# Optimization experiments

Hardware: AMD Instinct MI355X
Metric: run time of the kernel (lower is better)

Reference implementation:

```python
import jax, jax.numpy as jnp
import numpy as np

D_MODEL = 1024


def setup_inputs() -> dict:
    key = jax.random.key(0)
    ks = jax.random.split(key, 8)
    B, S, D = 32, 2048, D_MODEL
    scale = 1.0 / np.sqrt(D)
    return {
        "query": jax.random.normal(ks[0], (B, D), dtype=jnp.float32),
        "keys": jax.random.normal(ks[1], (B, S, D), dtype=jnp.float32),
        "Wq_w": jax.random.normal(ks[2], (D, D), dtype=jnp.float32) * scale,
        "Wq_b": jax.random.normal(ks[3], (D,), dtype=jnp.float32) * 0.01,
        "Wk_w": jax.random.normal(ks[4], (D, D), dtype=jnp.float32) * scale,
        "Wk_b": jax.random.normal(ks[5], (D,), dtype=jnp.float32) * 0.01,
        "v_w": jax.random.normal(ks[6], (D,), dtype=jnp.float32) * scale,
        "v_b": jax.random.normal(ks[7], (1,), dtype=jnp.float32) * 0.01,
    }


def reference(query, keys, Wq_w, Wq_b, Wk_w, Wk_b, v_w, v_b):
    # q: [B, 1, D], k: [B, S, D]
    q = (query @ Wq_w.T + Wq_b)[:, None, :]
    k = keys @ Wk_w.T + Wk_b
    # additive (Bahdanau) scores: [B, S]
    scores = jnp.einsum("bsd,d->bs", jnp.tanh(q + k), v_w) + v_b[0]
    attn = jax.nn.softmax(scores, axis=-1)
    # weighted sum over original keys: [B, D]
    context = jnp.einsum("bs,bsd->bd", attn, keys)
    return (context, attn)
```

## Files before the change

### kernel.cpp

```cpp
#include <hip/hip_runtime.h>
#include <cstddef>
#include <cstdint>

#define BATCH 32
#define SEQ 2048
#define DM 1024

typedef __attribute__((ext_vector_type(8))) _Float16 half8v;
typedef __attribute__((ext_vector_type(4))) _Float16 half4v;
typedef __attribute__((ext_vector_type(2))) __fp16 fp16x2;
typedef __attribute__((ext_vector_type(4))) float f32x4;

__device__ _Float16 g_Bpk[8 * 8 * 32 * 4 * 16 * 8];
__device__ float g_q[BATCH * DM];
__device__ float g_sp[8][BATCH * SEQ];

__device__ __forceinline__ float tanh_fast(float x) {
    float e = __expf(2.0f * x);
    return 1.0f - 2.0f / (e + 1.0f);
}

__global__ __launch_bounds__(256) void packb_kernel(const float* __restrict__ Wk_w) {
    int blk = blockIdx.x;
    int nc = blk >> 3, sub = blk & 7;
    int t = threadIdx.x;
    int row = t & 15, kgrp = (t >> 4) & 3, kt0 = t >> 6;
    const float* src = Wk_w + (size_t)(nc * 128 + sub * 16 + row) * DM;
    _Float16* dst = g_Bpk + (size_t)blk * 16384;
#pragma unroll
    for (int pass = 0; pass < 8; ++pass) {
        int kt = pass * 4 + kt0;
        float4 w0 = *reinterpret_cast<const float4*>(src + kt * 32 + kgrp * 8);
        float4 w1 = *reinterpret_cast<const float4*>(src + kt * 32 + kgrp * 8 + 4);
        union { _Float16 f[8]; half8v v; } h;
        h.f[0] = (_Float16)w0.x; h.f[1] = (_Float16)w0.y;
        h.f[2] = (_Float16)w0.z; h.f[3] = (_Float16)w0.w;
        h.f[4] = (_Float16)w1.x; h.f[5] = (_Float16)w1.y;
        h.f[6] = (_Float16)w1.z; h.f[7] = (_Float16)w1.w;
        *reinterpret_cast<half8v*>(&dst[(size_t)((kt * 4 + kgrp) * 16 + row) * 8]) = h.v;
    }
}

__global__ __launch_bounds__(256) void init_kernel(float* __restrict__ context) {
    int idx = blockIdx.x * 256 + threadIdx.x;
    if (idx < BATCH * DM) context[idx] = 0.f;
}

__global__ __launch_bounds__(256) void qproj_kernel(const float* __restrict__ query,
                                                    const float* __restrict__ Wq_w,
                                                    const float* __restrict__ Wq_b) {
    int d = blockIdx.x;
    int t = threadIdx.x;
    __shared__ float wrow[DM];
    __shared__ float part[8][32];
    reinterpret_cast<float4*>(wrow)[t] =
        reinterpret_cast<const float4*>(Wq_w + (size_t)d * DM)[t];
    __syncthreads();
    int b = t & 31, seg = t >> 5;
    const float4* qp = reinterpret_cast<const float4*>(query + b * DM + seg * 128);
    const float4* wp = reinterpret_cast<const float4*>(wrow + seg * 128);
    float acc = 0.f;
#pragma unroll
    for (int i = 0; i < 32; ++i) {
        float4 qv = qp[i];
        float4 wv = wp[i];
        acc += qv.x * wv.x + qv.y * wv.y + qv.z * wv.z + qv.w * wv.w;
    }
    part[seg][b] = acc;
    __syncthreads();
    if (t < 32) {
        float s = Wq_b[d];
#pragma unroll
        for (int g = 0; g < 8; ++g) s += part[g][t];
        g_q[t * DM + d] = s;
    }
}

#define BM 128
#define BN 256
#define NT2 16

__global__ __launch_bounds__(256, 2) void scores_kernel(const float* __restrict__ keys,
                                                        const float* __restrict__ Wk_b,
                                                        const float* __restrict__ v_w) {
    __shared__ _Float16 AhS[2][2][4][BM + 1][8];

    const unsigned bid = blockIdx.x;
    const unsigned L = (bid & 7u) * 256u + (bid >> 3);
    const int mtile = (int)(L >> 2);
    const int nchunk = (int)(L & 3u);
    const int m0 = mtile * BM;
    const int b = m0 >> 11;

    const int t = threadIdx.x;
    const int w = t >> 6, l = t & 63;
    const int wm = w >> 1, wn = w & 1;
    const int lr = l & 15, lg = l >> 4;

    const int akc = (l & 7) >> 1;
    const int aoff = ((l & 7) & 1) * 4;
    const float* Ap = keys + (size_t)(m0 + w * 32 + (l >> 3)) * DM + (l & 7) * 4;

    const int oldnc = nchunk * 2 + wn;
    const _Float16* Bp = g_Bpk + (size_t)oldnc * 8 * 16384
                               + (size_t)(l >> 4) * 128 + (size_t)(l & 15) * 8;

    float4 as0[4], as1[4];
    half8v bE[8], bO[8];

    f32x4 acc[4][8];
#pragma unroll
    for (int mi = 0; mi < 4; ++mi)
#pragma unroll
        for (int ni = 0; ni < 8; ++ni)
#pragma unroll
            for (int c = 0; c < 4; ++c) acc[mi][ni][c] = 0.f;

#define LOAD_A2(kt)                                                              \
    {                                                                            \
        _Pragma("unroll") for (int j = 0; j < 4; ++j)                            \
            as0[j] = *reinterpret_cast<const float4*>(                           \
                Ap + (size_t)j * 8 * DM + (kt) * 64);                            \
        _Pragma("unroll") for (int j = 0; j < 4; ++j)                            \
            as1[j] = *reinterpret_cast<const float4*>(                           \
                Ap + (size_t)j * 8 * DM + (kt) * 64 + 32);                       \
    }
#define LOAD_BF(ks, dst)                                                         \
    {                                                                            \
        _Pragma("unroll") for (int ni = 0; ni < 8; ++ni)                         \
            dst[ni] = *reinterpret_cast<const half8v*>(                          \
                Bp + (size_t)ni * 16384 + (size_t)(ks) * 512);                   \
    }
#define STAGE_ONE(bufi, sub, areg)                                               \
    {                                                                            \
        _Pragma("unroll") for (int j = 0; j < 4; ++j) {                          \
            const float* fa = reinterpret_cast<const float*>(&areg[j]);          \
            union { fp16x2 h2[2]; half4v v; } u;                                 \
            u.h2[0] = __builtin_amdgcn_cvt_pkrtz(fa[0], fa[1]);                  \
            u.h2[1] = __builtin_amdgcn_cvt_pkrtz(fa[2], fa[3]);                  \
            *reinterpret_cast<half4v*>(                                          \
                &AhS[bufi][sub][akc][w * 32 + j * 8 + (l >> 3)][aoff]) = u.v;    \
        }                                                                        \
    }
#define COMPUTE_S(bufi, sub, breg)                                               \
    {                                                                            \
        __builtin_amdgcn_s_setprio(1);                                           \
        _Pragma("unroll") for (int mi = 0; mi < 4; ++mi) {                       \
            half8v ahv = *reinterpret_cast<const half8v*>(                       \
                &AhS[bufi][sub][lg][wm * 64 + mi * 16 + lr][0]);                 \
            _Pragma("unroll") for (int ni = 0; ni < 8; ++ni)                     \
                acc[mi][ni] = __builtin_amdgcn_mfma_f32_16x16x32_f16(            \
                    ahv, breg[ni], acc[mi][ni], 0, 0, 0);                        \
        }                                                                        \
        __builtin_amdgcn_s_setprio(0);                                          \
    }
#define SYNC()                                                                   \
    asm volatile("s_waitcnt lgkmcnt(0)" ::: "memory");                           \
    __builtin_amdgcn_s_barrier();                                                \
    asm volatile("" ::: "memory");

    LOAD_A2(0);
    LOAD_BF(0, bE);
    STAGE_ONE(0, 0, as0);
    STAGE_ONE(0, 1, as1);
    SYNC()

    for (int tt = 0; tt < NT2; ++tt) {
        const int cb = tt & 1;
        LOAD_BF(2 * tt + 1, bO);
        if (tt + 1 < NT2) LOAD_A2(tt + 1);
        COMPUTE_S(cb, 0, bE);
        COMPUTE_S(cb, 1, bO);
        if (tt + 1 < NT2) {
            STAGE_ONE(cb ^ 1, 0, as0);
            STAGE_ONE(cb ^ 1, 1, as1);
            LOAD_BF(2 * tt + 2, bE);
        }
        SYNC()
    }

    float qb[8], vw[8];
#pragma unroll
    for (int ni = 0; ni < 8; ++ni) {
        int n = oldnc * 128 + ni * 16 + lr;
        qb[ni] = g_q[b * DM + n] + Wk_b[n];
        vw[ni] = v_w[n];
    }
#pragma unroll
    for (int mi = 0; mi < 4; ++mi) {
#pragma unroll
        for (int rg = 0; rg < 4; ++rg) {
            float p = 0.f;
#pragma unroll
            for (int ni = 0; ni < 8; ++ni) {
                float val = acc[mi][ni][rg] + qb[ni];
                p += tanh_fast(val) * vw[ni];
            }
#pragma unroll
            for (int off = 8; off >= 1; off >>= 1) p += __shfl_xor(p, off, 16);
            if (lr == 0)
                g_sp[oldnc][m0 + wm * 64 + mi * 16 + lg * 4 + rg] = p;
        }
    }
#undef LOAD_A2
#undef LOAD_BF
#undef STAGE_ONE
#undef COMPUTE_S
#undef SYNC
}

__global__ __launch_bounds__(256) void softmax_kernel(float* __restrict__ attn) {
    int b = blockIdx.x;
    int tid = threadIdx.x;
    __shared__ float redm[4];
    __shared__ float reds[4];
    float v[8];
    float mx = -1e30f;
#pragma unroll
    for (int i = 0; i < 8; ++i) {
        int idx = b * SEQ + i * 256 + tid;
        float s = 0.f;
#pragma unroll
        for (int pslot = 0; pslot < 8; ++pslot) s += g_sp[pslot][idx];
        v[i] = s;
        mx = fmaxf(mx, v[i]);
    }
#pragma unroll
    for (int off = 32; off >= 1; off >>= 1) mx = fmaxf(mx, __shfl_xor(mx, off));
    int wid = tid >> 6;
    if ((tid & 63) == 0) redm[wid] = mx;
    __syncthreads();
    mx = fmaxf(fmaxf(redm[0], redm[1]), fmaxf(redm[2], redm[3]));
    float sum = 0.f;
#pragma unroll
    for (int i = 0; i < 8; ++i) {
        v[i] = expf(v[i] - mx);
        sum += v[i];
    }
#pragma unroll
    for (int off = 32; off >= 1; off >>= 1) sum += __shfl_xor(sum, off);
    if ((tid & 63) == 0) reds[wid] = sum;
    __syncthreads();
    sum = reds[0] + reds[1] + reds[2] + reds[3];
    float inv = 1.f / sum;
#pragma unroll
    for (int i = 0; i < 8; ++i) attn[b * SEQ + i * 256 + tid] = v[i] * inv;
}

__global__ __launch_bounds__(256) void context_kernel(const float* __restrict__ keys,
                                                      const float* __restrict__ attn,
                                                      float* __restrict__ context) {
    int id = blockIdx.x;
    int schunk = id & 15;
    int b = id >> 4;
    int tid = threadIdx.x;
    __shared__ float a_s[128];
    if (tid < 128) a_s[tid] = attn[b * SEQ + schunk * 128 + tid];
    __syncthreads();
    const float4* kp =
        reinterpret_cast<const float4*>(keys + ((size_t)b * SEQ + schunk * 128) * DM) + tid;
    float4 acc = {0.f, 0.f, 0.f, 0.f};
#pragma unroll 4
    for (int s = 0; s < 128; ++s) {
        float4 kv = kp[(size_t)s * (DM / 4)];
        float a = a_s[s];
        acc.x += a * kv.x; acc.y += a * kv.y; acc.z += a * kv.z; acc.w += a * kv.w;
    }
    atomicAdd(&context[b * DM + tid * 4 + 0], acc.x);
    atomicAdd(&context[b * DM + tid * 4 + 1], acc.y);
    atomicAdd(&context[b * DM + tid * 4 + 2], acc.z);
    atomicAdd(&context[b * DM + tid * 4 + 3], acc.w);
}

extern "C" void kernel_launch(void* const* d_in, const int* in_sizes, int n_in,
                              void* d_out, int out_size, void* d_ws, size_t ws_size,
                              hipStream_t stream) {
    const float* query = (const float*)d_in[0];
    const float* keys  = (const float*)d_in[1];
    const float* Wq_w  = (const float*)d_in[2];
    const float* Wq_b  = (const float*)d_in[3];
    const float* Wk_w  = (const float*)d_in[4];
    const float* Wk_b  = (const float*)d_in[5];
    const float* v_w   = (const float*)d_in[6];

    float* context = (float*)d_out;
    float* attn    = context + BATCH * DM;

    hipLaunchKernelGGL(packb_kernel, dim3(64), dim3(256), 0, stream, Wk_w);
    hipLaunchKernelGGL(init_kernel, dim3(128), dim3(256), 0, stream, context);
    hipLaunchKernelGGL(qproj_kernel, dim3(DM), dim3(256), 0, stream, query, Wq_w, Wq_b);
    hipLaunchKernelGGL(scores_kernel, dim3((BATCH * SEQ / BM) * (DM / BN)), dim3(256), 0, stream,
                       keys, Wk_b, v_w);
    hipLaunchKernelGGL(softmax_kernel, dim3(BATCH), dim3(256), 0, stream, attn);
    hipLaunchKernelGGL(context_kernel, dim3(512), dim3(256), 0, stream, keys, attn, context);
}
```

Measured before the change: 236.9 us.

## Switch scores GEMM to 32x32x16 MFMA with repacked B layout

Replaces the 16x16x32 f16 MFMA tiles in the scores GEMM with 32x32x16 MFMA tiles, so each wave holds 2x4 accumulators of 16 floats instead of 4x8 of 4. The packed Wk layout, the LDS A layout and the epilogue row mapping are rewritten to match. B fragments are now four rotating register sets loaded in the gaps between compute steps. The aim is fewer LDS A reads per MFMA and a higher-throughput MFMA shape, at the cost of more B global loads per k-tile and a new epilogue shuffle pattern.

```diff
diff --git a/kernel.cpp b/kernel.cpp
--- a/kernel.cpp
+++ b/kernel.cpp
@@ -9,9 +9,9 @@
 typedef __attribute__((ext_vector_type(8))) _Float16 half8v;
 typedef __attribute__((ext_vector_type(4))) _Float16 half4v;
 typedef __attribute__((ext_vector_type(2))) __fp16 fp16x2;
-typedef __attribute__((ext_vector_type(4))) float f32x4;
-
-__device__ _Float16 g_Bpk[8 * 8 * 32 * 4 * 16 * 8];
+typedef __attribute__((ext_vector_type(16))) float f32x16;
+
+__device__ _Float16 g_Bpk[8 * 4 * 64 * 64 * 8];
 __device__ float g_q[BATCH * DM];
 __device__ float g_sp[8][BATCH * SEQ];
 
@@ -22,22 +22,27 @@
 
 __global__ __launch_bounds__(256) void packb_kernel(const float* __restrict__ Wk_w) {
     int blk = blockIdx.x;
-    int nc = blk >> 3, sub = blk & 7;
+    int oldnc = blk >> 3, kq = blk & 7;
     int t = threadIdx.x;
-    int row = t & 15, kgrp = (t >> 4) & 3, kt0 = t >> 6;
-    const float* src = Wk_w + (size_t)(nc * 128 + sub * 16 + row) * DM;
-    _Float16* dst = g_Bpk + (size_t)blk * 16384;
-#pragma unroll
-    for (int pass = 0; pass < 8; ++pass) {
-        int kt = pass * 4 + kt0;
-        float4 w0 = *reinterpret_cast<const float4*>(src + kt * 32 + kgrp * 8);
-        float4 w1 = *reinterpret_cast<const float4*>(src + kt * 32 + kgrp * 8 + 4);
-        union { _Float16 f[8]; half8v v; } h;
-        h.f[0] = (_Float16)w0.x; h.f[1] = (_Float16)w0.y;
-        h.f[2] = (_Float16)w0.z; h.f[3] = (_Float16)w0.w;
-        h.f[4] = (_Float16)w1.x; h.f[5] = (_Float16)w1.y;
-        h.f[6] = (_Float16)w1.z; h.f[7] = (_Float16)w1.w;
-        *reinterpret_cast<half8v*>(&dst[(size_t)((kt * 4 + kgrp) * 16 + row) * 8]) = h.v;
+    int w = t >> 6, l = t & 63;
+    int c32 = l & 31, khalf = l >> 5;
+#pragma unroll
+    for (int ni = 0; ni < 4; ++ni) {
+#pragma unroll
+        for (int s = 0; s < 2; ++s) {
+            int ks = kq * 8 + w * 2 + s;
+            const float* src = Wk_w + (size_t)(oldnc * 128 + ni * 32 + c32) * DM
+                             + ks * 16 + khalf * 8;
+            float4 f0 = *reinterpret_cast<const float4*>(src);
+            float4 f1 = *reinterpret_cast<const float4*>(src + 4);
+            union { fp16x2 h2[4]; half8v v; } u;
+            u.h2[0] = __builtin_amdgcn_cvt_pkrtz(f0.x, f0.y);
+            u.h2[1] = __builtin_amdgcn_cvt_pkrtz(f0.z, f0.w);
+            u.h2[2] = __builtin_amdgcn_cvt_pkrtz(f1.x, f1.y);
+            u.h2[3] = __builtin_amdgcn_cvt_pkrtz(f1.z, f1.w);
+            *reinterpret_cast<half8v*>(
+                &g_Bpk[(((size_t)(oldnc * 4 + ni) * 64 + ks) * 64 + l) * 8]) = u.v;
+        }
     }
 }
 
@@ -83,7 +88,7 @@
 __global__ __launch_bounds__(256, 2) void scores_kernel(const float* __restrict__ keys,
                                                         const float* __restrict__ Wk_b,
                                                         const float* __restrict__ v_w) {
-    __shared__ _Float16 AhS[2][2][4][BM + 1][8];
+    __shared__ _Float16 AhS[2][8][BM + 1][8];
 
     const unsigned bid = blockIdx.x;
     const unsigned L = (bid & 7u) * 256u + (bid >> 3);
@@ -95,26 +100,25 @@
     const int t = threadIdx.x;
     const int w = t >> 6, l = t & 63;
     const int wm = w >> 1, wn = w & 1;
-    const int lr = l & 15, lg = l >> 4;
+    const int c32 = l & 31, hi = l >> 5;
 
     const int akc = (l & 7) >> 1;
     const int aoff = ((l & 7) & 1) * 4;
     const float* Ap = keys + (size_t)(m0 + w * 32 + (l >> 3)) * DM + (l & 7) * 4;
 
     const int oldnc = nchunk * 2 + wn;
-    const _Float16* Bp = g_Bpk + (size_t)oldnc * 8 * 16384
-                               + (size_t)(l >> 4) * 128 + (size_t)(l & 15) * 8;
+    const _Float16* Bp = g_Bpk + (size_t)(oldnc * 4) * 32768 + (size_t)l * 8;
 
     float4 as0[4], as1[4];
-    half8v bE[8], bO[8];
-
-    f32x4 acc[4][8];
-#pragma unroll
-    for (int mi = 0; mi < 4; ++mi)
-#pragma unroll
-        for (int ni = 0; ni < 8; ++ni)
-#pragma unroll
-            for (int c = 0; c < 4; ++c) acc[mi][ni][c] = 0.f;
+    half8v bA[4], bB[4], bC[4], bD[4];
+
+    f32x16 acc[2][4];
+#pragma unroll
+    for (int mi = 0; mi < 2; ++mi)
+#pragma unroll
+        for (int ni = 0; ni < 4; ++ni)
+#pragma unroll
+            for (int c = 0; c < 16; ++c) acc[mi][ni][c] = 0.f;
 
 #define LOAD_A2(kt)                                                              \
     {                                                                            \
@@ -127,9 +131,9 @@
     }
 #define LOAD_BF(ks, dst)                                                         \
     {                                                                            \
-        _Pragma("unroll") for (int ni = 0; ni < 8; ++ni)                         \
+        _Pragma("unroll") for (int ni = 0; ni < 4; ++ni)                         \
             dst[ni] = *reinterpret_cast<const half8v*>(                          \
-                Bp + (size_t)ni * 16384 + (size_t)(ks) * 512);                   \
+                Bp + (size_t)ni * 32768 + (size_t)(ks) * 512);                   \
     }
 #define STAGE_ONE(bufi, sub, areg)                                               \
     {                                                                            \
@@ -139,18 +143,18 @@
             u.h2[0] = __builtin_amdgcn_cvt_pkrtz(fa[0], fa[1]);                  \
             u.h2[1] = __builtin_amdgcn_cvt_pkrtz(fa[2], fa[3]);                  \
             *reinterpret_cast<half4v*>(                                          \
-                &AhS[bufi][sub][akc][w * 32 + j * 8 + (l >> 3)][aoff]) = u.v;    \
+                &AhS[bufi][(sub) * 4 + akc][w * 32 + j * 8 + (l >> 3)][aoff]) = u.v; \
         }                                                                        \
     }
-#define COMPUTE_S(bufi, sub, breg)                                               \
+#define COMPUTE_S(bufi, step, bset)                                              \
     {                                                                            \
         __builtin_amdgcn_s_setprio(1);                                           \
-        _Pragma("unroll") for (int mi = 0; mi < 4; ++mi) {                       \
+        _Pragma("unroll") for (int mi = 0; mi < 2; ++mi) {                       \
             half8v ahv = *reinterpret_cast<const half8v*>(                       \
-                &AhS[bufi][sub][lg][wm * 64 + mi * 16 + lr][0]);                 \
-            _Pragma("unroll") for (int ni = 0; ni < 8; ++ni)                     \
-                acc[mi][ni] = __builtin_amdgcn_mfma_f32_16x16x32_f16(            \
-                    ahv, breg[ni], acc[mi][ni], 0, 0, 0);                        \
+                &AhS[bufi][(step) * 2 + hi][wm * 64 + mi * 32 + c32][0]);        \
+            _Pragma("unroll") for (int ni = 0; ni < 4; ++ni)                     \
+                acc[mi][ni] = __builtin_amdgcn_mfma_f32_32x32x16_f16(            \
+                    ahv, bset[ni], acc[mi][ni], 0, 0, 0);                        \
         }                                                                        \
         __builtin_amdgcn_s_setprio(0);                                          \
     }
@@ -160,46 +164,53 @@
     asm volatile("" ::: "memory");
 
     LOAD_A2(0);
-    LOAD_BF(0, bE);
+    LOAD_BF(0, bA);
+    LOAD_BF(1, bB);
     STAGE_ONE(0, 0, as0);
     STAGE_ONE(0, 1, as1);
     SYNC()
 
     for (int tt = 0; tt < NT2; ++tt) {
         const int cb = tt & 1;
-        LOAD_BF(2 * tt + 1, bO);
+        LOAD_BF(4 * tt + 2, bC);
         if (tt + 1 < NT2) LOAD_A2(tt + 1);
-        COMPUTE_S(cb, 0, bE);
-        COMPUTE_S(cb, 1, bO);
+        COMPUTE_S(cb, 0, bA);
+        LOAD_BF(4 * tt + 3, bD);
+        COMPUTE_S(cb, 1, bB);
         if (tt + 1 < NT2) {
             STAGE_ONE(cb ^ 1, 0, as0);
+            LOAD_BF(4 * tt + 4, bA);
+        }
+        COMPUTE_S(cb, 2, bC);
+        if (tt + 1 < NT2) {
             STAGE_ONE(cb ^ 1, 1, as1);
-            LOAD_BF(2 * tt + 2, bE);
+            LOAD_BF(4 * tt + 5, bB);
         }
+        COMPUTE_S(cb, 3, bD);
         SYNC()
     }
 
-    float qb[8], vw[8];
-#pragma unroll
-    for (int ni = 0; ni < 8; ++ni) {
-        int n = oldnc * 128 + ni * 16 + lr;
+    float qb[4], vw[4];
+#pragma unroll
+    for (int ni = 0; ni < 4; ++ni) {
+        int n = oldnc * 128 + ni * 32 + c32;
         qb[ni] = g_q[b * DM + n] + Wk_b[n];
         vw[ni] = v_w[n];
     }
 #pragma unroll
-    for (int mi = 0; mi < 4; ++mi) {
-#pragma unroll
-        for (int rg = 0; rg < 4; ++rg) {
+    for (int mi = 0; mi < 2; ++mi) {
+#pragma unroll
+        for (int r = 0; r < 16; ++r) {
             float p = 0.f;
 #pragma unroll
-            for (int ni = 0; ni < 8; ++ni) {
-                float val = acc[mi][ni][rg] + qb[ni];
+            for (int ni = 0; ni < 4; ++ni) {
+                float val = acc[mi][ni][r] + qb[ni];
                 p += tanh_fast(val) * vw[ni];
             }
 #pragma unroll
-            for (int off = 8; off >= 1; off >>= 1) p += __shfl_xor(p, off, 16);
-            if (lr == 0)
-                g_sp[oldnc][m0 + wm * 64 + mi * 16 + lg * 4 + rg] = p;
+            for (int off = 16; off >= 1; off >>= 1) p += __shfl_xor(p, off);
+            if (c32 == 0)
+                g_sp[oldnc][m0 + wm * 64 + mi * 32 + (r & 3) + 8 * (r >> 2) + 4 * hi] = p;
         }
     }
 #undef LOAD_A2
```

New measurement: 250.3 us. 5.6% more time.
